# Performance work log

Hardware: AMD Instinct MI355X
Metric: run time of the kernel (lower is better)

Reference implementation:

```python
import jax, jax.numpy as jnp
import numpy as np

N_JOINTS = 17
NEG_INF = -9e15
BN_EPS = 1e-5


def _chain_adjacency(n):
    # skeleton-like chain adjacency with self loops (stand-in for the pose skeleton adj)
    a = np.eye(n, dtype=np.float32)
    idx = np.arange(n - 1)
    a[idx, idx + 1] = 1.0
    a[idx + 1, idx] = 1.0
    return jnp.asarray(a)


def setup_inputs() -> dict:
    key = jax.random.key(0)
    ks = jax.random.split(key, 6)
    B, D, T, N = 32, 128, 512, N_JOINTS
    H, hd = 16, D // 16  # 16 heads, head_dim 8
    s = 1.0 / np.sqrt(D)
    return {
        "x": jax.random.normal(ks[0], (B, D, T, N), dtype=jnp.float32),
        "adj": _chain_adjacency(N),
        "Wq": jax.random.normal(ks[1], (H, D, hd), dtype=jnp.float32) * s,
        "Wk": jax.random.normal(ks[2], (H, D, hd), dtype=jnp.float32) * s,
        "Wv": jax.random.normal(ks[3], (H, D, hd), dtype=jnp.float32) * s,
        "adj2": jnp.full((H, N, N), 1e-6, dtype=jnp.float32),
        "conv_w": jax.random.normal(ks[4], (2 * D, 2 * D), dtype=jnp.float32) * (1.0 / np.sqrt(2 * D)),
        "bn_gamma": jnp.ones((2 * D,), dtype=jnp.float32),
        "bn_beta": jnp.zeros((2 * D,), dtype=jnp.float32),
        "bn_mean": jnp.zeros((2 * D,), dtype=jnp.float32),
        "bn_var": jnp.ones((2 * D,), dtype=jnp.float32),
    }


def reference(x, adj, Wq, Wk, Wv, adj2, conv_w, bn_gamma, bn_beta, bn_mean, bn_var):
    hd = Wq.shape[-1]
    xp = jnp.transpose(x, (0, 2, 3, 1))                      # (B,T,N,D)
    # multi-head adjacency-masked graph attention (MultiGlobalGraph)
    q = jnp.einsum('btnd,hde->bhtne', xp, Wq)
    k = jnp.einsum('btnd,hde->bhtne', xp, Wk)
    v = jnp.einsum('btnd,hde->bhtne', xp, Wv)
    e = jnp.einsum('bhtne,bhtme->bhtnm', q, k) / jnp.sqrt(jnp.asarray(hd, xp.dtype))
    a = adj[None, :, :] + adj2                               # (H,N,N) learnable adj offset
    a = 0.5 * (a + jnp.swapaxes(a, -1, -2))                  # symmetrize
    mask = a > 0
    e = jnp.where(mask[None, :, None, :, :], e, jnp.asarray(NEG_INF, e.dtype))
    attn = jax.nn.softmax(e, axis=-1)                        # (B,H,T,N,N)
    out = jnp.einsum('bhtnm,bhtme->bhtne', attn, v)
    B, H, T, N, _ = out.shape
    out = jnp.transpose(out, (0, 2, 3, 1, 4)).reshape(B, T, N, H * hd)
    # residual concat + conv1x1 + BN(eval) + ReLU
    cat = jnp.concatenate([xp, out], axis=-1)                # (B,T,N,2D)
    y = jnp.einsum('btnc,oc->btno', cat, conv_w)
    y = (y - bn_mean) * jax.lax.rsqrt(bn_var + BN_EPS) * bn_gamma + bn_beta
    y = jax.nn.relu(y)
    return jnp.transpose(y, (0, 3, 1, 2))                    # (B,2D,T,N)
```

## Files before the change

### kernel.cpp

```cpp
#include <hip/hip_runtime.h>
#include <hip/hip_bf16.h>
#include <math.h>

#define NJ 17
#define DD 128
#define TT 512
#define HH 16
#define CC 256
#define NEG_INF -9e15f

typedef __attribute__((ext_vector_type(8))) short short8;
typedef __attribute__((ext_vector_type(4))) float floatx4;
typedef _Float16 h8 __attribute__((ext_vector_type(8)));

#define WB_CONV 0
#define WB_QKV  131072
#define WB_MOFF 229376
#define WB_BIAS 247872
#define PREP_ITEMS (65536 + 49152 + 4624 + 256)

__global__ __launch_bounds__(256) void prep_kernel(
        const float* __restrict__ adj,
        const float* __restrict__ wq,
        const float* __restrict__ wk,
        const float* __restrict__ wv,
        const float* __restrict__ adj2,
        const float* __restrict__ conv_w,
        const float* __restrict__ gamma,
        const float* __restrict__ beta,
        const float* __restrict__ mean,
        const float* __restrict__ var,
        char* __restrict__ ws) {
    int g = blockIdx.x * 256 + threadIdx.x;
    if (g < 65536) {
        int j = g & 7, lane = (g >> 3) & 63, kn = g >> 9;
        int ks = kn & 7, nt = kn >> 3;
        int o = nt * 16 + (lane & 15);
        int c = ks * 32 + ((lane >> 4) & 3) * 8 + j;
        float sg = gamma[o] * rsqrtf(var[o] + 1e-5f);
        ((__hip_bfloat16*)(ws + WB_CONV))[g] = __float2bfloat16(conv_w[o * CC + c] * sg);
        return;
    }
    g -= 65536;
    if (g < 49152) {
        int j = g & 7, lane = (g >> 3) & 63, kn = g >> 9;
        int ks = kn & 3, nt = kn >> 2;
        int n = nt * 16 + (lane & 15);
        int k = ks * 32 + ((lane >> 4) & 3) * 8 + j;
        int mat = n >> 7;
        int wcol = n & 127;
        int h = wcol >> 3, e = wcol & 7;
        const float* src = (mat == 0) ? wq : ((mat == 1) ? wk : wv);
        float v = src[(h * DD + k) * 8 + e];
        if (mat == 0) v *= 0.35355339059327373f;
        ((__hip_bfloat16*)(ws + WB_QKV))[g] = __float2bfloat16(v);
        return;
    }
    g -= 49152;
    if (g < HH * NJ * NJ) {
        int h = g / (NJ * NJ);
        int r = g - h * NJ * NJ;
        int n = r / NJ, m = r - n * NJ;
        float a1 = adj[n * NJ + m] + adj2[(h * NJ + n) * NJ + m];
        float a2 = adj[m * NJ + n] + adj2[(h * NJ + m) * NJ + n];
        ((float*)(ws + WB_MOFF))[g] = (0.5f * (a1 + a2) > 0.f) ? 0.f : NEG_INF;
        return;
    }
    g -= HH * NJ * NJ;
    if (g < CC) {
        float sg = gamma[g] * rsqrtf(var[g] + 1e-5f);
        ((float*)(ws + WB_BIAS))[g] = beta[g] - mean[g] * sg;
    }
}

__global__ __launch_bounds__(256, 4) void gab_main(
        const float* __restrict__ x,
        const char* __restrict__ ws,
        float* __restrict__ out) {
    const int tp = blockIdx.x;
    const int t0 = 2 * ((tp & 7) * 32 + (tp >> 3));
    const int b = blockIdx.y;
    const int tid = threadIdx.x;
    const int lane = tid & 63;
    const int wave = tid >> 6;
    const int l15 = lane & 15;
    const int lq = lane >> 4;

    __shared__ __align__(16) __hip_bfloat16 cat[48][264];
    __shared__ __align__(16) _Float16 qkv[3][34][128];

    const float* xb = x + (size_t)b * DD * TT * NJ + (size_t)t0 * NJ;
    for (int i = tid; i < DD * 17; i += 256) {
        int d = i / 17;
        int j = 2 * (i - d * 17);
        float2 f = *(const float2*)(xb + (size_t)d * (TT * NJ) + j);
        cat[j][d] = __float2bfloat16(f.x);
        cat[j + 1][d] = __float2bfloat16(f.y);
    }
    {
        uint4 z = make_uint4(0, 0, 0, 0);
        for (int i = tid; i < 448; i += 256) {
            int r = 34 + (i >> 5);
            int c16 = i & 31;
            *(uint4*)((char*)&cat[r][0] + c16 * 16) = z;
        }
    }
    __syncthreads();

    {
        const short8* bbase = (const short8*)(ws + WB_QKV);
        const int nt0 = wave * 6;
        for (int i = 0; i < 6; ++i) {
            const int nt = nt0 + i;
            floatx4 acc0 = {0.f, 0.f, 0.f, 0.f}, acc1 = acc0, acc2 = acc0;
            const short8* bp = bbase + (nt * 4) * 64 + lane;
#pragma unroll
            for (int ks = 0; ks < 4; ++ks) {
                short8 bf = bp[ks * 64];
                const int k0 = ks * 32 + lq * 8;
                short8 a0 = *(const short8*)&cat[l15][k0];
                short8 a1 = *(const short8*)&cat[16 + l15][k0];
                short8 a2 = *(const short8*)&cat[32 + l15][k0];
                acc0 = __builtin_amdgcn_mfma_f32_16x16x32_bf16(a0, bf, acc0, 0, 0, 0);
                acc1 = __builtin_amdgcn_mfma_f32_16x16x32_bf16(a1, bf, acc1, 0, 0, 0);
                acc2 = __builtin_amdgcn_mfma_f32_16x16x32_bf16(a2, bf, acc2, 0, 0, 0);
            }
            const int col = nt * 16 + l15;
            const int mat = col >> 7;
            const int mc = col & 127;
            const int rbase = lq * 4;
#pragma unroll
            for (int r = 0; r < 4; ++r) {
                qkv[mat][rbase + r][mc] = (_Float16)acc0[r];
                qkv[mat][16 + rbase + r][mc] = (_Float16)acc1[r];
                int row2 = 32 + rbase + r;
                if (row2 < 34) qkv[mat][row2][mc] = (_Float16)acc2[r];
            }
        }
    }
    __syncthreads();

    for (int it = tid; it < 2 * HH * NJ; it += 256) {
        const int t = it / (HH * NJ);
        const int r2 = it - t * (HH * NJ);
        const int h = r2 / NJ;
        const int n = r2 - h * NJ;
        const float* mo = (const float*)(ws + WB_MOFF) + (h * NJ + n) * NJ;
        const h8 qv = *(const h8*)&qkv[0][t * NJ + n][h * 8];
        float s[NJ];
        float mx = -3.4e38f;
#pragma unroll
        for (int m = 0; m < NJ; ++m) {
            const h8 kv = *(const h8*)&qkv[1][t * NJ + m][h * 8];
            float a = mo[m];
#pragma unroll
            for (int e = 0; e < 8; ++e) a += (float)qv[e] * (float)kv[e];
            s[m] = a;
            mx = fmaxf(mx, a);
        }
        float sum = 0.f;
#pragma unroll
        for (int m = 0; m < NJ; ++m) {
            float p = __expf(s[m] - mx);
            s[m] = p;
            sum += p;
        }
        const float inv = 1.0f / sum;
        float ov[8];
#pragma unroll
        for (int e = 0; e < 8; ++e) ov[e] = 0.f;
#pragma unroll
        for (int m = 0; m < NJ; ++m) {
            const h8 vv = *(const h8*)&qkv[2][t * NJ + m][h * 8];
            const float p = s[m];
#pragma unroll
            for (int e = 0; e < 8; ++e) ov[e] += p * (float)vv[e];
        }
        const int row = t * NJ + n;
#pragma unroll
        for (int e = 0; e < 8; ++e)
            cat[row][128 + h * 8 + e] = __float2bfloat16(ov[e] * inv);
    }
    __syncthreads();

    {
        const short8* cbase = (const short8*)(ws + WB_CONV);
        const float* biasp = (const float*)(ws + WB_BIAS);
        const int nt0 = wave * 4;
        for (int i = 0; i < 4; ++i) {
            const int nt = nt0 + i;
            floatx4 acc0 = {0.f, 0.f, 0.f, 0.f}, acc1 = acc0, acc2 = acc0;
            const short8* bp = cbase + (nt * 8) * 64 + lane;
#pragma unroll
            for (int ks = 0; ks < 8; ++ks) {
                short8 bf = bp[ks * 64];
                const int k0 = ks * 32 + lq * 8;
                short8 a0 = *(const short8*)&cat[l15][k0];
                short8 a1 = *(const short8*)&cat[16 + l15][k0];
                short8 a2 = *(const short8*)&cat[32 + l15][k0];
                acc0 = __builtin_amdgcn_mfma_f32_16x16x32_bf16(a0, bf, acc0, 0, 0, 0);
                acc1 = __builtin_amdgcn_mfma_f32_16x16x32_bf16(a1, bf, acc1, 0, 0, 0);
                acc2 = __builtin_amdgcn_mfma_f32_16x16x32_bf16(a2, bf, acc2, 0, 0, 0);
            }
            const int o = nt * 16 + l15;
            const float bias = biasp[o];
            const size_t ob = ((size_t)b * CC + o) * (TT * NJ) + (size_t)t0 * NJ;
            const int rbase = lq * 4;
#pragma unroll
            for (int r = 0; r < 4; ++r) {
                out[ob + rbase + r] = fmaxf(acc0[r] + bias, 0.f);
                out[ob + 16 + rbase + r] = fmaxf(acc1[r] + bias, 0.f);
                int row2 = 32 + rbase + r;
                if (row2 < 34) out[ob + row2] = fmaxf(acc2[r] + bias, 0.f);
            }
        }
    }
}

extern "C" void kernel_launch(void* const* d_in, const int* in_sizes, int n_in,
                              void* d_out, int out_size, void* d_ws, size_t ws_size,
                              hipStream_t stream) {
    const float* x      = (const float*)d_in[0];
    const float* adj    = (const float*)d_in[1];
    const float* wq     = (const float*)d_in[2];
    const float* wk     = (const float*)d_in[3];
    const float* wv     = (const float*)d_in[4];
    const float* adj2   = (const float*)d_in[5];
    const float* conv_w = (const float*)d_in[6];
    const float* gamma  = (const float*)d_in[7];
    const float* beta   = (const float*)d_in[8];
    const float* mean   = (const float*)d_in[9];
    const float* var    = (const float*)d_in[10];
    char* ws   = (char*)d_ws;
    float* outp = (float*)d_out;

    const int B = in_sizes[0] / (DD * TT * NJ);

    prep_kernel<<<(PREP_ITEMS + 255) / 256, 256, 0, stream>>>(
        adj, wq, wk, wv, adj2, conv_w, gamma, beta, mean, var, ws);

    dim3 grid(TT / 2, B);
    gab_main<<<grid, 256, 0, stream>>>(x, ws, outp);
}
```

Baseline: 637.7 us.

## Alias Q into cat buffer, use 512-thread blocks and fdot2 attention

Q is now written into the unused upper half of the cat rows, and the padding rows and the separate Q buffer are dropped. This cuts shared memory per block so more blocks can be resident. The block grows to 512 threads, so each wave handles half as many QKV and conv output tiles. The attention score dot products use packed fp16 fdot2, and the attention output is written with one vector store. The trade-off is that MFMA loads of rows 34-47 now read stale data from the K/V region instead of zeros; those rows feed only discarded outputs.

```diff
diff --git a/kernel.cpp b/kernel.cpp
--- a/kernel.cpp
+++ b/kernel.cpp
@@ -12,6 +12,7 @@
 typedef __attribute__((ext_vector_type(8))) short short8;
 typedef __attribute__((ext_vector_type(4))) float floatx4;
 typedef _Float16 h8 __attribute__((ext_vector_type(8)));
+typedef _Float16 h2 __attribute__((ext_vector_type(2)));
 
 #define WB_CONV 0
 #define WB_QKV  131072
@@ -73,7 +74,11 @@
     }
 }
 
-__global__ __launch_bounds__(256, 4) void gab_main(
+#define CAT_STRIDE 264
+#define LDS_CAT_BYTES (34 * CAT_STRIDE * 2)
+#define LDS_TOTAL (LDS_CAT_BYTES + 2 * 34 * 128 * 2)
+
+__global__ __launch_bounds__(512, 6) void gab_main(
         const float* __restrict__ x,
         const char* __restrict__ ws,
         float* __restrict__ out) {
@@ -86,31 +91,24 @@
     const int l15 = lane & 15;
     const int lq = lane >> 4;
 
-    __shared__ __align__(16) __hip_bfloat16 cat[48][264];
-    __shared__ __align__(16) _Float16 qkv[3][34][128];
+    __shared__ __align__(16) char smem[LDS_TOTAL];
+    __hip_bfloat16 (*cat)[CAT_STRIDE] = (__hip_bfloat16 (*)[CAT_STRIDE])smem;
+    _Float16 (*kv)[34][128] = (_Float16 (*)[34][128])(smem + LDS_CAT_BYTES);
 
     const float* xb = x + (size_t)b * DD * TT * NJ + (size_t)t0 * NJ;
-    for (int i = tid; i < DD * 17; i += 256) {
+    for (int i = tid; i < DD * 17; i += 512) {
         int d = i / 17;
         int j = 2 * (i - d * 17);
         float2 f = *(const float2*)(xb + (size_t)d * (TT * NJ) + j);
         cat[j][d] = __float2bfloat16(f.x);
         cat[j + 1][d] = __float2bfloat16(f.y);
     }
-    {
-        uint4 z = make_uint4(0, 0, 0, 0);
-        for (int i = tid; i < 448; i += 256) {
-            int r = 34 + (i >> 5);
-            int c16 = i & 31;
-            *(uint4*)((char*)&cat[r][0] + c16 * 16) = z;
-        }
-    }
     __syncthreads();
 
     {
         const short8* bbase = (const short8*)(ws + WB_QKV);
-        const int nt0 = wave * 6;
-        for (int i = 0; i < 6; ++i) {
+        const int nt0 = wave * 3;
+        for (int i = 0; i < 3; ++i) {
             const int nt = nt0 + i;
             floatx4 acc0 = {0.f, 0.f, 0.f, 0.f}, acc1 = acc0, acc2 = acc0;
             const short8* bp = bbase + (nt * 4) * 64 + lane;
@@ -129,65 +127,90 @@
             const int mat = col >> 7;
             const int mc = col & 127;
             const int rbase = lq * 4;
-#pragma unroll
-            for (int r = 0; r < 4; ++r) {
-                qkv[mat][rbase + r][mc] = (_Float16)acc0[r];
-                qkv[mat][16 + rbase + r][mc] = (_Float16)acc1[r];
-                int row2 = 32 + rbase + r;
-                if (row2 < 34) qkv[mat][row2][mc] = (_Float16)acc2[r];
+            if (mat == 0) {
+                _Float16* qd = (_Float16*)smem + 128 + mc;
+#pragma unroll
+                for (int r = 0; r < 4; ++r) {
+                    qd[(rbase + r) * CAT_STRIDE] = (_Float16)acc0[r];
+                    qd[(16 + rbase + r) * CAT_STRIDE] = (_Float16)acc1[r];
+                    int row2 = 32 + rbase + r;
+                    if (row2 < 34) qd[row2 * CAT_STRIDE] = (_Float16)acc2[r];
+                }
+            } else {
+                _Float16* kd = &kv[mat - 1][0][mc];
+#pragma unroll
+                for (int r = 0; r < 4; ++r) {
+                    kd[(rbase + r) * 128] = (_Float16)acc0[r];
+                    kd[(16 + rbase + r) * 128] = (_Float16)acc1[r];
+                    int row2 = 32 + rbase + r;
+                    if (row2 < 34) kd[row2 * 128] = (_Float16)acc2[r];
+                }
             }
         }
     }
     __syncthreads();
 
-    for (int it = tid; it < 2 * HH * NJ; it += 256) {
-        const int t = it / (HH * NJ);
-        const int r2 = it - t * (HH * NJ);
-        const int h = r2 / NJ;
-        const int n = r2 - h * NJ;
-        const float* mo = (const float*)(ws + WB_MOFF) + (h * NJ + n) * NJ;
-        const h8 qv = *(const h8*)&qkv[0][t * NJ + n][h * 8];
-        float s[NJ];
-        float mx = -3.4e38f;
-#pragma unroll
-        for (int m = 0; m < NJ; ++m) {
-            const h8 kv = *(const h8*)&qkv[1][t * NJ + m][h * 8];
-            float a = mo[m];
-#pragma unroll
-            for (int e = 0; e < 8; ++e) a += (float)qv[e] * (float)kv[e];
-            s[m] = a;
-            mx = fmaxf(mx, a);
+    {
+        const float* moff = (const float*)(ws + WB_MOFF);
+        for (int it = tid; it < 2 * HH * NJ; it += 512) {
+            const int t = it / (HH * NJ);
+            const int r2 = it - t * (HH * NJ);
+            const int h = r2 / NJ;
+            const int n = r2 - h * NJ;
+            const int row = t * NJ + n;
+            const float* mo = moff + (h * NJ + n) * NJ;
+            const h8 qv = *(const h8*)((const _Float16*)smem + row * CAT_STRIDE + 128 + h * 8);
+            const h2* q2 = (const h2*)&qv;
+            float s[NJ];
+            float mx = -3.4e38f;
+#pragma unroll
+            for (int m = 0; m < NJ; ++m) {
+                const h8 kvec = *(const h8*)&kv[0][t * NJ + m][h * 8];
+                float a = mo[m];
+#if __has_builtin(__builtin_amdgcn_fdot2)
+                const h2* k2 = (const h2*)&kvec;
+                a = __builtin_amdgcn_fdot2(q2[0], k2[0], a, false);
+                a = __builtin_amdgcn_fdot2(q2[1], k2[1], a, false);
+                a = __builtin_amdgcn_fdot2(q2[2], k2[2], a, false);
+                a = __builtin_amdgcn_fdot2(q2[3], k2[3], a, false);
+#else
+#pragma unroll
+                for (int e = 0; e < 8; ++e) a += (float)qv[e] * (float)kvec[e];
+#endif
+                s[m] = a;
+                mx = fmaxf(mx, a);
+            }
+            float sum = 0.f;
+#pragma unroll
+            for (int m = 0; m < NJ; ++m) {
+                float p = __expf(s[m] - mx);
+                s[m] = p;
+                sum += p;
+            }
+            const float inv = 1.0f / sum;
+            float ov[8];
+#pragma unroll
+            for (int e = 0; e < 8; ++e) ov[e] = 0.f;
+#pragma unroll
+            for (int m = 0; m < NJ; ++m) {
+                const h8 vvec = *(const h8*)&kv[1][t * NJ + m][h * 8];
+                const float p = s[m];
+#pragma unroll
+                for (int e = 0; e < 8; ++e) ov[e] += p * (float)vvec[e];
+            }
+            __hip_bfloat16 tmp[8];
+#pragma unroll
+            for (int e = 0; e < 8; ++e) tmp[e] = __float2bfloat16(ov[e] * inv);
+            *(short8*)((__hip_bfloat16*)smem + row * CAT_STRIDE + 128 + h * 8) = *(short8*)tmp;
         }
-        float sum = 0.f;
-#pragma unroll
-        for (int m = 0; m < NJ; ++m) {
-            float p = __expf(s[m] - mx);
-            s[m] = p;
-            sum += p;
-        }
-        const float inv = 1.0f / sum;
-        float ov[8];
-#pragma unroll
-        for (int e = 0; e < 8; ++e) ov[e] = 0.f;
-#pragma unroll
-        for (int m = 0; m < NJ; ++m) {
-            const h8 vv = *(const h8*)&qkv[2][t * NJ + m][h * 8];
-            const float p = s[m];
-#pragma unroll
-            for (int e = 0; e < 8; ++e) ov[e] += p * (float)vv[e];
-        }
-        const int row = t * NJ + n;
-#pragma unroll
-        for (int e = 0; e < 8; ++e)
-            cat[row][128 + h * 8 + e] = __float2bfloat16(ov[e] * inv);
     }
     __syncthreads();
 
     {
         const short8* cbase = (const short8*)(ws + WB_CONV);
         const float* biasp = (const float*)(ws + WB_BIAS);
-        const int nt0 = wave * 4;
-        for (int i = 0; i < 4; ++i) {
+        const int nt0 = wave * 2;
+        for (int i = 0; i < 2; ++i) {
             const int nt = nt0 + i;
             floatx4 acc0 = {0.f, 0.f, 0.f, 0.f}, acc1 = acc0, acc2 = acc0;
             const short8* bp = cbase + (nt * 8) * 64 + lane;
@@ -240,5 +263,5 @@
         adj, wq, wk, wv, adj2, conv_w, gamma, beta, mean, var, ws);
 
     dim3 grid(TT / 2, B);
-    gab_main<<<grid, 256, 0, stream>>>(x, ws, outp);
+    gab_main<<<grid, 512, 0, stream>>>(x, ws, outp);
 }
```

Result: slower. 852.0 us (+33.6%).
